# Performance work log

Measured on AMD Instinct MI355X. Metric: run time of the kernel, lower is better.

The kernel has to match this reference:

```python
import jax, jax.numpy as jnp
import numpy as np
from math import comb

N_DERIV = 4          # num_derivatives
ODE_DIM = 512        # ode_dimension
K = ODE_DIM * (N_DERIV + 1)


def _build_system(n, d):
    # system_matrices_1d: A_1d = flip(pascal), Q_1d = flip(hilbert), chol(Q_1d)
    x = np.arange(n + 1)
    B = np.array([[comb(i, j) for j in range(n + 1)] for i in range(n + 1)], dtype=np.float64)
    A1 = B[::-1, ::-1]                                  # flip both axes
    Hil = 1.0 / (x[:, None] + x[None, :] + 1.0)
    Q1 = Hil[::-1, ::-1]
    L1 = np.linalg.cholesky(Q1)
    a = np.kron(np.eye(d), A1)
    q = np.kron(np.eye(d), L1)
    return jnp.asarray(a, jnp.float32), jnp.asarray(q, jnp.float32)


def _qr_r(x):
    # sqrtm_to_cholesky: upper-triangular factor from reduced QR
    return jnp.linalg.qr(x)[1]


def setup_inputs() -> dict:
    key = jax.random.key(0)
    k1, k2, k3, k4, k5 = jax.random.split(key, 5)
    a, q_sqrtm_lower = _build_system(N_DERIV, ODE_DIM)
    m0 = jax.random.normal(k1, (K,), dtype=jnp.float32)
    l0 = jnp.tril(jax.random.normal(k2, (K, K), dtype=jnp.float32) * 0.05)
    H = jax.random.normal(k3, (ODE_DIM, K), dtype=jnp.float32) * 0.1
    bias = jax.random.normal(k4, (ODE_DIM,), dtype=jnp.float32)
    dt = jax.random.uniform(k5, (1,), dtype=jnp.float32, minval=0.05, maxval=0.15)
    return {"m0": m0, "l0": l0, "H": H, "bias": bias, "dt": dt,
            "a": a, "q_sqrtm_lower": q_sqrtm_lower}


def reference(m0, l0, H, bias, dt, a, q_sqrtm_lower):
    d = H.shape[0]
    k = m0.shape[0]
    n1 = k // d                       # num_derivatives + 1
    # --- assemble_preconditioner ---
    powers = jnp.arange(n1 - 1, -1, -1, dtype=m0.dtype)
    scales = jnp.exp(jax.lax.lgamma(powers + 1.0))
    pw = powers + 0.5
    adt = jnp.abs(dt[0])
    p = jnp.tile(adt ** pw / scales, d)          # (k,)
    p_inv = jnp.tile(adt ** (-pw) * scales, d)   # (k,)
    # --- extrapolate_mean ---
    m0_p = p_inv * m0
    m_ext_p = a @ m0_p
    m_ext = p * m_ext_p
    # EK-style linearized observation residual
    m_obs = H @ m_ext - bias                     # (d,)
    # --- estimate_error ---
    l_obs_ns_e = H @ (p_inv[:, None] * q_sqrtm_lower)            # (d,k)
    l_obs_raw = _qr_r(l_obs_ns_e.T).T                            # lower (d,d)
    res_white = jax.scipy.linalg.solve_triangular(l_obs_raw.T, m_obs, lower=False)
    diffusion = jnp.sqrt(jnp.dot(res_white, res_white) / res_white.size)
    error = diffusion * jnp.sqrt(jnp.einsum('nj,nj->n', l_obs_raw, l_obs_raw))
    # --- complete_extrapolation (sum_of_sqrtm_factors) ---
    R1 = (a @ (p_inv[:, None] * l0)).T           # (k,k)
    R2 = (diffusion * q_sqrtm_lower).T           # (k,k)
    l_ext_p = _qr_r(jnp.vstack([R1, R2])).T      # lower (k,k)
    l_ext = p[:, None] * l_ext_p
    # --- final_correction ---
    l_obs_ns = H @ l_ext                         # (d,k)
    l_obs = _qr_r(l_obs_ns.T).T                  # lower (d,d)
    crosscov = l_ext @ l_obs_ns.T                # (k,d)
    gain = jax.scipy.linalg.cho_solve((l_obs, True), crosscov.T).T  # (k,d)
    m_cor = m_ext - gain @ m_obs
    l_cor = l_ext - gain @ l_obs_ns
    u = jnp.reshape(m_cor, (-1, d), order='F')[0]  # derivative-0 block
    return m_cor, l_cor, u, error, diffusion
```

## Files before the change

### kernel.cpp

```cpp
#include <hip/hip_runtime.h>
#include <math.h>

#define KDIM 2560
#define DDIM 512
#define NB 64

#define QM 2560
#define QM2 1024
#define QN 512
#define PW 32
#define UW 3
#define QACT 544

#define OUT_LCOR 2560
#define OUT_U    6556160
#define OUT_ERR  6556672
#define OUT_DIFF 6557184


__global__ void k_setup(const float* dt, double* scal){
  if (threadIdx.x==0 && blockIdx.x==0){
    double adt = fabs((double)dt[0]);
    const double scales[5] = {24.0,6.0,2.0,1.0,1.0};
    for (int i=0;i<5;i++){
      double pw = (double)(4-i)+0.5;
      scal[i]   = pow(adt, pw)/scales[i];
      scal[5+i] = pow(adt,-pw)*scales[i];
    }
  }
}

__global__ __launch_bounds__(256) void k_mext_mobs(const float* a, const float* m0, const float* H,
                                                   const float* bias, const double* scal,
                                                   double* mext, double* mobs){
  __shared__ double me[KDIM];
  __shared__ double red[256];
  double pp[5], pv[5];
  #pragma unroll
  for (int i=0;i<5;i++){ pp[i]=scal[i]; pv[i]=scal[5+i]; }
  int tid=threadIdx.x;
  for (int r=tid; r<KDIM; r+=256){
    int j=r/5, i=r%5;
    const float* arow = a + (size_t)r*KDIM + 5*j;
    const float* m0b  = m0 + 5*j;
    double acc=0;
    #pragma unroll
    for (int l=0;l<5;l++) acc += (double)arow[l]*pv[l]*(double)m0b[l];
    me[r] = pp[i]*acc;
  }
  __syncthreads();
  if (blockIdx.x==0) for (int r=tid;r<KDIM;r+=256) mext[r]=me[r];
  int b = blockIdx.x;
  const float* Hr = H + (size_t)b*KDIM;
  double acc=0;
  for (int c=tid;c<KDIM;c+=256) acc += (double)Hr[c]*me[c];
  red[tid]=acc; __syncthreads();
  for (int s=128;s>0;s>>=1){ if (tid<s) red[tid]+=red[tid+s]; __syncthreads(); }
  if (tid==0) mobs[b] = red[0] - (double)bias[b];
}

__global__ void k_A2(const float* H, const float* q, const double* scal,
                     double* Atop, double* Abot){
  int idx = blockIdx.x*blockDim.x+threadIdx.x;
  if (idx >= QN*QM) return;
  double pv[5];
  #pragma unroll
  for (int t=0;t<5;t++) pv[t]=scal[5+t];
  int j = idx / QM;
  int i = idx % QM;
  int bi = i/5;
  double acc=0;
  #pragma unroll
  for (int t=0;t<5;t++)
    acc += (double)H[(size_t)j*QM + 5*bi+t]*pv[t]*(double)q[(size_t)(5*bi+t)*QM + i];
  if (i < 512) Atop[(size_t)j*QM2 + i] = acc;
  else         Abot[(size_t)j*2048 + (i-512)] = acc;
}

__global__ void k_copyB(const double* Gbot, double* AQ){
  int idx = blockIdx.x*blockDim.x+threadIdx.x;
  if (idx >= 512*512) return;
  int c = idx/512, rr = idx%512;
  AQ[(size_t)c*QM2 + 512 + rr] = (rr<=c) ? Gbot[(size_t)c*512 + rr] : 0.0;
}

__global__ __launch_bounds__(576) void qr_panel(double* A, double* vhead, int col0, double* Tbuf){
  __shared__ double redw[9][PW];
  __shared__ double rednorm[9];
  __shared__ double sh[3];
  __shared__ double wsh[PW];
  __shared__ double alphas[PW], betas[PW];
  __shared__ double VtVs[PW][PW];
  __shared__ double Tsh[PW][PW];
  int tid=threadIdx.x, wid=tid>>6, lane=tid&63;
  int m = QM2 - col0; if (m > QACT) m = QACT;
  bool on = tid < m;
  double x[PW];
  #pragma unroll
  for (int j=0;j<PW;j++)
    x[j] = on ? A[(size_t)(col0+j)*QM2 + col0 + tid] : 0.0;
  for (int j=0;j<PW;j++){
    double v0 = (tid>=j && on)? x[j] : 0.0;
    double ps = v0*v0;
    #pragma unroll
    for (int o=32;o>0;o>>=1) ps += __shfl_down(ps,o);
    if (lane==0) rednorm[wid]=ps;
    if (tid==j) sh[0]=x[j];
    __syncthreads();
    if (tid==0){
      double s0=0;
      for (int t=0;t<9;t++) s0+=rednorm[t];
      double x1=sh[0];
      double nrm=sqrt(s0);
      double alpha=(x1>=0.0)?-nrm:nrm;
      double v1=x1-alpha;
      double vtv=s0-2.0*alpha*x1+alpha*alpha;
      double b=(vtv>0.0)?2.0/vtv:0.0;
      sh[1]=v1; sh[2]=b;
      alphas[j]=alpha; betas[j]=b;
      vhead[col0+j]=v1;
    }
    __syncthreads();
    if (tid==j) x[j]=sh[1];
    double b=sh[2];
    double v=(tid>=j && on)? x[j] : 0.0;
    #pragma unroll
    for (int t=0;t<PW;t++){
      if (t==j) continue;
      double p=v*x[t];
      #pragma unroll
      for (int o=32;o>0;o>>=1) p+=__shfl_down(p,o);
      if (lane==0) redw[wid][t]=p;
    }
    __syncthreads();
    if (tid<PW && tid!=j){
      double tot=0;
      #pragma unroll
      for (int t2=0;t2<9;t2++) tot+=redw[t2][tid];
      if (tid>j) wsh[tid]=b*tot;
      else       VtVs[tid][j]=tot;
    }
    __syncthreads();
    if (v!=0.0){
      for (int t=j+1;t<PW;t++) x[t]-=wsh[t]*v;
    }
  }
  __syncthreads();
  if (tid<PW){
    int i=tid;
    Tsh[i][i]=betas[i];
    for (int j2=i+1;j2<PW;j2++){
      double z=0;
      for (int t=i;t<j2;t++) z+=Tsh[i][t]*VtVs[t][j2];
      Tsh[i][j2]=-betas[j2]*z;
    }
  }
  __syncthreads();
  for (int e=tid;e<PW*PW;e+=576){
    int i=e/PW, j2=e%PW;
    Tbuf[e] = (j2>=i)? Tsh[i][j2] : 0.0;
  }
  if (on){
    #pragma unroll
    for (int j=0;j<PW;j++)
      A[(size_t)(col0+j)*QM2 + col0 + tid] = (tid==j)? alphas[j] : x[j];
  }
}

__global__ __launch_bounds__(256) void qr_update(double* A, const double* vhead,
                                                 const double* Tbuf, int col0){
  __shared__ double redu[4][PW];
  __shared__ double ysh[PW];
  __shared__ double wsh[PW];
  int tid=threadIdx.x, wid=tid>>6, lane=tid&63;
  int cc=col0+PW+blockIdx.x;
  int m=QM2-col0; if (m > QACT) m = QACT;
  double a[UW];
  #pragma unroll
  for (int w=0;w<UW;w++){
    int lr=tid+w*256;
    a[w]=(lr<m)? A[(size_t)cc*QM2+col0+lr] : 0.0;
  }
  double acc[PW];
  #pragma unroll
  for (int j=0;j<PW;j++) acc[j]=0;
  #pragma unroll
  for (int w=0;w<UW;w++){
    int lr=tid+w*256;
    if (lr<m){
      #pragma unroll
      for (int j=0;j<PW;j++){
        double vj;
        if (lr>j)       vj=A[(size_t)(col0+j)*QM2+col0+lr];
        else if (lr==j) vj=vhead[col0+j];
        else            vj=0.0;
        acc[j]+=vj*a[w];
      }
    }
  }
  #pragma unroll
  for (int j=0;j<PW;j++){
    double d=acc[j];
    #pragma unroll
    for (int o=32;o>0;o>>=1) d+=__shfl_down(d,o);
    if (lane==0) redu[wid][j]=d;
  }
  __syncthreads();
  if (tid<PW){
    double y=0;
    #pragma unroll
    for (int t=0;t<4;t++) y+=redu[t][tid];
    ysh[tid]=y;
  }
  __syncthreads();
  if (tid<PW){
    double s=0;
    for (int t=0;t<=tid;t++) s+=Tbuf[t*PW+tid]*ysh[t];
    wsh[tid]=s;
  }
  __syncthreads();
  #pragma unroll
  for (int w=0;w<UW;w++){
    int lr=tid+w*256;
    if (lr<m){
      double s=0;
      #pragma unroll
      for (int j=0;j<PW;j++){
        double vj;
        if (lr>j)       vj=A[(size_t)(col0+j)*QM2+col0+lr];
        else if (lr==j) vj=vhead[col0+j];
        else            vj=0.0;
        s+=vj*wsh[j];
      }
      A[(size_t)cc*QM2+col0+lr]=a[w]-s;
    }
  }
}

__global__ __launch_bounds__(512) void k_rpost(const double* Aq, const double* mobs,
                                               double* scal, float* out){
  __shared__ double b[DDIM];
  __shared__ double xs[DDIM];
  __shared__ double D[NB][NB+1];
  __shared__ double red[DDIM];
  __shared__ double g1sh[DDIM];
  int tid=threadIdx.x;
  {
    double s=0;
    for (int r=0;r<=tid;r++){ double v=Aq[(size_t)tid*QM2 + r]; s+=v*v; }
    g1sh[tid]=s;
  }
  b[tid]=mobs[tid];
  __syncthreads();
  for (int p=7;p>=0;p--){
    int b0=p*NB;
    for (int e=tid;e<NB*NB;e+=512){ int i=e&63, j2=e>>6; D[i][j2]=Aq[(size_t)(b0+j2)*QM2 + b0+i]; }
    __syncthreads();
    if (tid<64){
      double bi=b[b0+tid];
      for (int k=NB-1;k>=0;k--){
        double bk=__shfl(bi,k);
        double xk=bk/D[k][k];
        if (tid<k) bi-=D[tid][k]*xk;
        if (tid==k) bi=xk;
      }
      xs[b0+tid]=bi;
    }
    __syncthreads();
    if (tid<b0){
      double s=0;
      #pragma unroll 8
      for (int j2=0;j2<NB;j2++) s+=Aq[(size_t)(b0+j2)*QM2 + tid]*xs[b0+j2];
      b[tid]-=s;
    }
    __syncthreads();
  }
  red[tid]=xs[tid]*xs[tid]; __syncthreads();
  for (int s=256;s>0;s>>=1){ if (tid<s) red[tid]+=red[tid+s]; __syncthreads(); }
  double diff=sqrt(red[0]/(double)DDIM);
  if (tid==0){ scal[10]=diff; out[OUT_DIFF]=(float)diff; }
  out[OUT_ERR+tid]=(float)(diff*sqrt(fmax(g1sh[tid],0.0)));
}

__global__ void k_X(const float* a, const float* l0, const double* scal, float* X){
  int idx=blockIdx.x*blockDim.x+threadIdx.x;
  if (idx>=KDIM*KDIM) return;
  double pv[5];
  #pragma unroll
  for (int t=0;t<5;t++) pv[t]=scal[5+t];
  int r=idx/KDIM, c=idx%KDIM;
  int j=r/5;
  const float* arow = a + (size_t)r*KDIM + 5*j;
  double acc=0;
  #pragma unroll
  for (int l=0;l<5;l++)
    acc += (double)arow[l]*pv[l]*(double)l0[(size_t)(5*j+l)*KDIM+c];
  X[idx]=(float)acc;
}

template<typename TA,int ATR,typename TB,int BTR,int MODE>
__global__ __launch_bounds__(256) void gemm64(const TA* __restrict__ A,int lda,
                                              const TB* __restrict__ B,int ldb,
                                              void* __restrict__ Cv,int ldc,
                                              int K,int kmode){
  __shared__ double As[16][65];
  __shared__ double Bs[16][65];
  int tid=threadIdx.x, tx=tid&15, ty=tid>>4;
  int n0=blockIdx.x*64, m0=blockIdx.y*64;
  int ks=0, ke=K;
  if (kmode==1) ks=n0;
  else if (kmode==2) ke=min(K,n0+64);
  else if (kmode==3) ke=min(K,m0+64);
  else if (kmode==4) ks=m0;
  double acc[4][4]={};
  for (int k0=ks;k0<ke;k0+=16){
    if (ATR){
      for (int e=tid;e<16*64;e+=256){int k=e>>6,mm=e&63; As[k][mm]=(double)A[(size_t)(k0+k)*lda+m0+mm];}
    } else {
      for (int e=tid;e<64*16;e+=256){int mm=e>>4,k=e&15; As[k][mm]=(double)A[(size_t)(m0+mm)*lda+k0+k];}
    }
    if (BTR){
      for (int e=tid;e<64*16;e+=256){int nn=e>>4,k=e&15; Bs[k][nn]=(double)B[(size_t)(n0+nn)*ldb+k0+k];}
    } else {
      for (int e=tid;e<16*64;e+=256){int k=e>>6,nn=e&63; Bs[k][nn]=(double)B[(size_t)(k0+k)*ldb+n0+nn];}
    }
    __syncthreads();
    #pragma unroll
    for (int t=0;t<16;t++){
      double av[4],bv[4];
      #pragma unroll
      for (int i=0;i<4;i++){av[i]=As[t][ty+16*i];bv[i]=Bs[t][tx+16*i];}
      #pragma unroll
      for (int i=0;i<4;i++)
        #pragma unroll
        for (int j=0;j<4;j++) acc[i][j]+=av[i]*bv[j];
    }
    __syncthreads();
  }
  #pragma unroll
  for (int i=0;i<4;i++){
    #pragma unroll
    for (int j=0;j<4;j++){
      size_t idx=(size_t)(m0+ty+16*i)*ldc+n0+tx+16*j;
      if (MODE==0) ((double*)Cv)[idx]=acc[i][j];
      else if (MODE==1) ((double*)Cv)[idx]-=acc[i][j];
      else ((float*)Cv)[idx]=(float)acc[i][j];
    }
  }
}

__global__ __launch_bounds__(256) void syrk_lower(const float* __restrict__ X, const float* __restrict__ q,
                                                  const double* __restrict__ scal,
                                                  double* __restrict__ G, int n){
  int t = blockIdx.x;
  int u = (int)((sqrtf(8.0f*(float)t+1.0f)+1.0f)*0.5f);
  while ((u*(u-1))/2 > t) u--;
  while ((u*(u+1))/2 <= t) u++;
  int s = (KDIM/64) - u;
  int r = s + (t - (u*(u-1))/2);
  int S0=s*64, R0=r*64;
  __shared__ double As[16][65];
  __shared__ double Bs[16][65];
  int tid=threadIdx.x, tx=tid&15, ty=tid>>4;
  int kend=min(n, S0+80);
  double acc[4][4]={};
  for (int k0=0;k0<kend;k0+=16){
    for (int e=tid;e<64*16;e+=256){int mm=e>>4,k=e&15; As[k][mm]=(double)X[(size_t)(R0+mm)*n+k0+k];}
    for (int e=tid;e<64*16;e+=256){int nn=e>>4,k=e&15; Bs[k][nn]=(double)X[(size_t)(S0+nn)*n+k0+k];}
    __syncthreads();
    #pragma unroll
    for (int t2=0;t2<16;t2++){
      double av[4],bv[4];
      #pragma unroll
      for (int i=0;i<4;i++){av[i]=As[t2][ty+16*i];bv[i]=Bs[t2][tx+16*i];}
      #pragma unroll
      for (int i=0;i<4;i++)
        #pragma unroll
        for (int j=0;j<4;j++) acc[i][j]+=av[i]*bv[j];
    }
    __syncthreads();
  }
  double dd = scal[10]*scal[10];
  #pragma unroll
  for (int i=0;i<4;i++)
    #pragma unroll
    for (int j=0;j<4;j++){
      int rr=R0+ty+16*i, c=S0+tx+16*j;
      double v=acc[i][j];
      if (c<=rr && (rr/5)==(c/5)){
        double qq=0;
        #pragma unroll
        for (int k=0;k<5;k++) qq += (double)q[(size_t)(rr%5)*KDIM+k]*(double)q[(size_t)(c%5)*KDIM+k];
        v += dd*qq;
      }
      G[(size_t)rr*n+c]=v;
    }
}

__global__ __launch_bounds__(256) void chol_diag(double* A, int n, int k0){
  __shared__ double P[NB][NB+1];
  int tid=threadIdx.x;
  for (int e=tid;e<NB*NB;e+=256){int r=e>>6,c=e&63;P[r][c]=A[(size_t)(k0+r)*n+k0+c];}
  int tx=tid&15, ty=tid>>4;
  __syncthreads();
  for (int j=0;j<NB;j++){
    double pj=P[j][j];
    __syncthreads();
    double rpj=1.0/sqrt(fmax(pj,1e-280));
    if (tid>j && tid<NB) P[tid][j]*=rpj;
    if (tid==j) P[j][j]=sqrt(fmax(pj,1e-280));
    __syncthreads();
    #pragma unroll
    for (int a2=0;a2<4;a2++){
      int r=ty+16*a2;
      double lrj=P[r][j];
      #pragma unroll
      for (int b2=0;b2<4;b2++){
        int c=tx+16*b2;
        if (r>j && c>j && c<=r) P[r][c]-=lrj*P[c][j];
      }
    }
    __syncthreads();
  }
  for (int e=tid;e<NB*NB;e+=256){int r=e>>6,c=e&63;A[(size_t)(k0+r)*n+k0+c]=P[r][c];}
}

__global__ __launch_bounds__(256) void chol_trsm(double* A,int n,int k0){
  __shared__ double Ls[NB][NB+1];
  __shared__ double St[NB][NB+1];
  __shared__ double rec[NB];
  int tid=threadIdx.x;
  for (int e=tid;e<NB*NB;e+=256){int r=e>>6,c=e&63;Ls[r][c]=A[(size_t)(k0+r)*n+k0+c];}
  __syncthreads();
  if (tid<NB) rec[tid]=1.0/Ls[tid][tid];
  int base=k0+NB+blockIdx.x*256;
  int myrow=base+tid;
  int mychunk=tid>>6, lrow=tid&63;
  double ar[NB];
  for (int ch=0;ch<4;ch++){
    int r0=base+ch*64;
    for (int e=tid;e<NB*NB;e+=256){
      int r=e>>6,c=e&63;
      if (r0+r<n) St[r][c]=A[(size_t)(r0+r)*n+k0+c];
    }
    __syncthreads();
    if (mychunk==ch && myrow<n){
      #pragma unroll
      for (int c=0;c<NB;c++) ar[c]=St[lrow][c];
    }
    __syncthreads();
  }
  if (myrow<n){
    #pragma unroll
    for (int j=0;j<NB;j++){
      double s=ar[j];
      #pragma unroll
      for (int t=0;t<j;t++) s-=ar[t]*Ls[j][t];
      ar[j]=s*rec[j];
    }
  }
  for (int ch=0;ch<4;ch++){
    int r0=base+ch*64;
    if (mychunk==ch && myrow<n){
      #pragma unroll
      for (int c=0;c<NB;c++) St[lrow][c]=ar[c];
    }
    __syncthreads();
    for (int e=tid;e<NB*NB;e+=256){
      int r=e>>6,c=e&63;
      if (r0+r<n) A[(size_t)(r0+r)*n+k0+c]=St[r][c];
    }
    __syncthreads();
  }
}

__global__ __launch_bounds__(256) void chol_syrk_fd(double* A,int n,int k0){
  int ts0=k0+NB;
  int t=blockIdx.x;
  int r=(int)((sqrtf(8.0f*(float)t+1.0f)-1.0f)*0.5f);
  while ((r*(r+1))/2 > t) r--;
  while (((r+1)*(r+2))/2 <= t) r++;
  int s=t-(r*(r+1))/2;
  int S0=ts0+s*64, R0=ts0+r*64;
  __shared__ double As[16][65];
  __shared__ double Bs[16][65];
  __shared__ double P[NB][NB+1];
  int tid=threadIdx.x, tx=tid&15, ty=tid>>4;
  double acc[4][4]={};
  for (int k0i=0;k0i<NB;k0i+=16){
    for (int e=tid;e<64*16;e+=256){int mm=e>>4,k=e&15; As[k][mm]=A[(size_t)(R0+mm)*n+k0+k0i+k];}
    for (int e=tid;e<64*16;e+=256){int nn=e>>4,k=e&15; Bs[k][nn]=A[(size_t)(S0+nn)*n+k0+k0i+k];}
    __syncthreads();
    #pragma unroll
    for (int tt=0;tt<16;tt++){
      double av[4],bv[4];
      #pragma unroll
      for (int i=0;i<4;i++){av[i]=As[tt][ty+16*i];bv[i]=Bs[tt][tx+16*i];}
      #pragma unroll
      for (int i=0;i<4;i++)
        #pragma unroll
        for (int j=0;j<4;j++) acc[i][j]+=av[i]*bv[j];
    }
    __syncthreads();
  }
  if (t!=0){
    #pragma unroll
    for (int i=0;i<4;i++)
      #pragma unroll
      for (int j=0;j<4;j++)
        A[(size_t)(R0+ty+16*i)*n+S0+tx+16*j]-=acc[i][j];
    return;
  }
  #pragma unroll
  for (int i=0;i<4;i++)
    #pragma unroll
    for (int j=0;j<4;j++)
      P[ty+16*i][tx+16*j] = A[(size_t)(R0+ty+16*i)*n+S0+tx+16*j] - acc[i][j];
  __syncthreads();
  for (int j=0;j<NB;j++){
    double pj=P[j][j];
    __syncthreads();
    double rpj=1.0/sqrt(fmax(pj,1e-280));
    if (tid>j && tid<NB) P[tid][j]*=rpj;
    if (tid==j) P[j][j]=sqrt(fmax(pj,1e-280));
    __syncthreads();
    #pragma unroll
    for (int a2=0;a2<4;a2++){
      int r2=ty+16*a2;
      double lrj=P[r2][j];
      #pragma unroll
      for (int b2=0;b2<4;b2++){
        int c=tx+16*b2;
        if (r2>j && c>j && c<=r2) P[r2][c]-=lrj*P[c][j];
      }
    }
    __syncthreads();
  }
  for (int e=tid;e<NB*NB;e+=256){int r2=e>>6,c=e&63;A[(size_t)(ts0+r2)*n+ts0+c]=P[r2][c];}
}

__global__ void k_extract(const double* G2, const double* scal, float* lext){
  int idx=blockIdx.x*blockDim.x+threadIdx.x;
  if (idx>=KDIM*KDIM) return;
  int r=idx/KDIM, c=idx%KDIM;
  double v = (c<=r)? scal[r%5]*G2[idx] : 0.0;
  lext[idx]=(float)v;
}

__global__ __launch_bounds__(256) void trinv_diag(const double* S, double* Linv){
  __shared__ double Ls[NB][NB+1];
  __shared__ double Ti[NB][NB+1];
  int jb=blockIdx.x, tid=threadIdx.x;
  for (int e=tid; e<DDIM*NB; e+=256){
    int r=e/NB, c=e%NB;
    Linv[(size_t)r*DDIM + jb*NB + c]=0.0;
  }
  for (int e=tid;e<NB*NB;e+=256){int r=e>>6,c=e&63; Ls[r][c]=S[(size_t)(jb*NB+r)*DDIM + jb*NB+c];}
  __syncthreads();
  if (tid<NB){
    int c=tid;
    for (int r=c;r<NB;r++){
      double s=(r==c)?1.0:0.0;
      for (int t=c;t<r;t++) s-=Ls[r][t]*Ti[t][c];
      Ti[r][c]=s/Ls[r][r];
    }
    for (int r=0;r<c;r++) Ti[r][c]=0.0;
  }
  __syncthreads();
  for (int e=tid;e<NB*NB;e+=256){int r=e>>6,c=e&63; Linv[(size_t)(jb*NB+r)*DDIM + jb*NB+c]=Ti[r][c];}
}

__global__ __launch_bounds__(256) void trinv_step(const double* S, double* Linv, int d){
  __shared__ double As[16][65];
  __shared__ double Bs[16][65];
  __shared__ double Ps[NB][NB+1];
  int jb=blockIdx.x, ib=jb+d;
  int tid=threadIdx.x, tx=tid&15, ty=tid>>4;
  double acc[4][4]={};
  int kstart=jb*NB, kend=ib*NB;
  for (int k0=kstart;k0<kend;k0+=16){
    for (int e=tid;e<64*16;e+=256){int mm=e>>4,k=e&15; As[k][mm]=S[(size_t)(ib*NB+mm)*DDIM + k0+k];}
    for (int e=tid;e<16*64;e+=256){int k=e>>6,nn=e&63; Bs[k][nn]=Linv[(size_t)(k0+k)*DDIM + jb*NB+nn];}
    __syncthreads();
    #pragma unroll
    for (int t=0;t<16;t++){
      double av[4],bv[4];
      #pragma unroll
      for (int i=0;i<4;i++){av[i]=As[t][ty+16*i];bv[i]=Bs[t][tx+16*i];}
      #pragma unroll
      for (int i=0;i<4;i++)
        #pragma unroll
        for (int j=0;j<4;j++) acc[i][j]+=av[i]*bv[j];
    }
    __syncthreads();
  }
  #pragma unroll
  for (int i=0;i<4;i++)
    #pragma unroll
    for (int j=0;j<4;j++) Ps[ty+16*i][tx+16*j]=acc[i][j];
  double o[4][4]={};
  __syncthreads();
  for (int k0=0;k0<NB;k0+=16){
    for (int e=tid;e<64*16;e+=256){int mm=e>>4,k=e&15; As[k][mm]=Linv[(size_t)(ib*NB+mm)*DDIM + ib*NB+k0+k];}
    __syncthreads();
    #pragma unroll
    for (int t=0;t<16;t++){
      double av[4],bv[4];
      #pragma unroll
      for (int i=0;i<4;i++){av[i]=As[t][ty+16*i];bv[i]=Ps[k0+t][tx+16*i];}
      #pragma unroll
      for (int i=0;i<4;i++)
        #pragma unroll
        for (int j=0;j<4;j++) o[i][j]+=av[i]*bv[j];
    }
    __syncthreads();
  }
  #pragma unroll
  for (int i=0;i<4;i++)
    #pragma unroll
    for (int j=0;j<4;j++)
      Linv[(size_t)(ib*NB+ty+16*i)*DDIM + jb*NB+tx+16*j] = -o[i][j];
}

__global__ void k_mcor(const double* Z, const double* mobs, const double* mext, float* out){
  __shared__ double mo[DDIM];
  for (int s=threadIdx.x;s<DDIM;s+=256) mo[s]=mobs[s];
  __syncthreads();
  int r=blockIdx.x*256+threadIdx.x;
  if (r>=KDIM) return;
  double acc=0;
  for (int s=0;s<DDIM;s++) acc += Z[(size_t)s*KDIM+r]*mo[s];
  double mc = mext[r]-acc;
  out[r]=(float)mc;
  if (r%5==0) out[OUT_U + r/5]=(float)mc;
}

__global__ __launch_bounds__(256) void k_lcor(const double* __restrict__ Z, const float* __restrict__ lobs,
                                              const float* __restrict__ lext, float* __restrict__ out){
  __shared__ double As[16][65];
  __shared__ double Bs[16][65];
  int tid=threadIdx.x, tx=tid&15, ty=tid>>4;
  int n0=blockIdx.x*64, m0=blockIdx.y*64;
  double acc[4][4]={};
  for (int k0=0;k0<DDIM;k0+=16){
    for (int e=tid;e<16*64;e+=256){int k=e>>6,mm=e&63; As[k][mm]=Z[(size_t)(k0+k)*KDIM+m0+mm];}
    for (int e=tid;e<16*64;e+=256){int k=e>>6,nn=e&63; Bs[k][nn]=(double)lobs[(size_t)(k0+k)*KDIM+n0+nn];}
    __syncthreads();
    #pragma unroll
    for (int t=0;t<16;t++){
      double av[4],bv[4];
      #pragma unroll
      for (int i=0;i<4;i++){av[i]=As[t][ty+16*i];bv[i]=Bs[t][tx+16*i];}
      #pragma unroll
      for (int i=0;i<4;i++)
        #pragma unroll
        for (int j=0;j<4;j++) acc[i][j]+=av[i]*bv[j];
    }
    __syncthreads();
  }
  #pragma unroll
  for (int i=0;i<4;i++)
    #pragma unroll
    for (int j=0;j<4;j++){
      size_t idx=(size_t)(m0+ty+16*i)*KDIM+n0+tx+16*j;
      out[OUT_LCOR+idx]=(float)((double)lext[idx]-acc[i][j]);
    }
}

extern "C" void kernel_launch(void* const* d_in, const int* in_sizes, int n_in,
                              void* d_out, int out_size, void* d_ws, size_t ws_size,
                              hipStream_t stream) {
  const float* m0  = (const float*)d_in[0];
  const float* l0  = (const float*)d_in[1];
  const float* H   = (const float*)d_in[2];
  const float* bias= (const float*)d_in[3];
  const float* dt  = (const float*)d_in[4];
  const float* a   = (const float*)d_in[5];
  const float* q   = (const float*)d_in[6];
  float* out = (float*)d_out;

  char* w=(char*)d_ws;
  auto alloc=[&](size_t bytes)->char*{ char* p=w; w += ((bytes+255)/256)*256; return p; };
  double* scal  =(double*)alloc(16*8);
  double* mext  =(double*)alloc((size_t)KDIM*8);
  double* mobs  =(double*)alloc((size_t)DDIM*8);
  double* vheadA=(double*)alloc((size_t)QN*8);
  double* Tbuf  =(double*)alloc((size_t)PW*PW*8);
  double* AQ    =(double*)alloc((size_t)QM2*QN*8);
  double* S     =(double*)alloc((size_t)DDIM*DDIM*8);
  double* G2    =(double*)alloc((size_t)KDIM*KDIM*8);
  float*  LOBS  =(float*) alloc((size_t)DDIM*KDIM*4);
  float*  X     =(float*) alloc((size_t)KDIM*KDIM*4);
  float*  LEXT  = X;
  double* Abot  = G2;
  double* Gbot  = Abot + (size_t)2048*512;
  double* Linv  = G2;
  double* C2    = Linv + (size_t)DDIM*DDIM;
  double* Y     = C2   + (size_t)DDIM*KDIM;
  double* Z     = Y    + (size_t)DDIM*KDIM;

  auto chol_full=[&](double* M, int n){
    chol_diag<<<1,256,0,stream>>>(M, n, 0);
    for (int k0=0;k0+NB<n;k0+=NB){
      int m = n-k0-NB;
      chol_trsm<<<(m+255)/256,256,0,stream>>>(M,n,k0);
      int T = m/64;
      chol_syrk_fd<<<T*(T+1)/2,256,0,stream>>>(M,n,k0);
    }
  };

  k_setup<<<1,1,0,stream>>>(dt, scal);
  k_mext_mobs<<<DDIM,256,0,stream>>>(a, m0, H, bias, scal, mext, mobs);

  k_A2<<<(QN*QM+255)/256,256,0,stream>>>(H, q, scal, AQ, Abot);
  gemm64<double,0,double,1,0><<<dim3(8,8),256,0,stream>>>(Abot,2048, Abot,2048, Gbot,512, 2048, 0);
  chol_full(Gbot, 512);
  k_copyB<<<(512*512+255)/256,256,0,stream>>>(Gbot, AQ);
  for (int p=0;p<QN/PW;p++){
    int col0=p*PW;
    qr_panel<<<1,576,0,stream>>>(AQ, vheadA, col0, Tbuf);
    int ntr = QN - col0 - PW;
    if (ntr>0) qr_update<<<ntr,256,0,stream>>>(AQ, vheadA, Tbuf, col0);
  }
  k_rpost<<<1,512,0,stream>>>(AQ, mobs, scal, out);

  k_X<<<(KDIM*KDIM+255)/256,256,0,stream>>>(a, l0, scal, X);
  syrk_lower<<<(KDIM/64)*((KDIM/64)+1)/2,256,0,stream>>>(X, q, scal, G2, KDIM);
  chol_full(G2, KDIM);
  k_extract<<<(KDIM*KDIM+255)/256,256,0,stream>>>(G2, scal, LEXT);

  gemm64<float,0,float,0,2><<<dim3(KDIM/64,DDIM/64),256,0,stream>>>(H,KDIM, LEXT,KDIM, LOBS,KDIM, KDIM, 1);
  gemm64<float,0,float,1,0><<<dim3(DDIM/64,DDIM/64),256,0,stream>>>(LOBS,KDIM, LOBS,KDIM, S,DDIM, KDIM, 0);
  chol_full(S, DDIM);
  trinv_diag<<<8,256,0,stream>>>(S, Linv);
  for (int d=1;d<8;d++)
    trinv_step<<<8-d,256,0,stream>>>(S, Linv, d);
  gemm64<float,0,float,1,0><<<dim3(KDIM/64,DDIM/64),256,0,stream>>>(LOBS,KDIM, LEXT,KDIM, C2,KDIM, KDIM, 2);
  gemm64<double,0,double,0,0><<<dim3(KDIM/64,DDIM/64),256,0,stream>>>(Linv,DDIM, C2,KDIM, Y,KDIM, DDIM, 3);
  gemm64<double,1,double,0,0><<<dim3(KDIM/64,DDIM/64),256,0,stream>>>(Linv,DDIM, Y,KDIM, Z,KDIM, DDIM, 4);

  k_mcor<<<(KDIM+255)/256,256,0,stream>>>(Z, mobs, mext, out);
  k_lcor<<<dim3(KDIM/64,KDIM/64),256,0,stream>>>(Z, LOBS, LEXT, out);
}
```

Before: 18.24 ms.

## Fuse blocked QR panel with lookahead trailing update into one launch per step

Replaces the separate qr_panel and qr_update launches with a single qr_step kernel. Block 0 applies the previous panel's reflectors to the next panel and then factors it, while the other blocks update the remaining trailing columns from the previous step, so the panel factorization overlaps with the trailing update. The panel width is halved to 16, which doubles the number of steps but makes each serial panel cheaper. Per-step T factors are kept in a Tbufs array, and the Cholesky syrk kernel gains a fuse flag that is always set to 1, so its behaviour is unchanged.

```diff
diff --git a/kernel.cpp b/kernel.cpp
--- a/kernel.cpp
+++ b/kernel.cpp
@@ -8,9 +8,8 @@
 #define QM 2560
 #define QM2 1024
 #define QN 512
-#define PW 32
-#define UW 3
-#define QACT 544
+#define PW 16
+#define QACT 528
 
 #define OUT_LCOR 2560
 #define OUT_U    6556160
@@ -84,7 +83,60 @@
   AQ[(size_t)c*QM2 + 512 + rr] = (rr<=c) ? Gbot[(size_t)c*512 + rr] : 0.0;
 }
 
-__global__ __launch_bounds__(576) void qr_panel(double* A, double* vhead, int col0, double* Tbuf){
+__global__ __launch_bounds__(576) void qr_step(double* A, double* vhead, double* Tbufs, int p){
+  int col0 = p*PW;
+  int tid=threadIdx.x, wid=tid>>6, lane=tid&63;
+
+  if (blockIdx.x > 0){
+    int pc0 = col0 - PW;
+    const double* T = Tbufs + (size_t)(p-1)*PW*PW;
+    int cc = col0 + PW + ((int)blockIdx.x - 1);
+    int m = QM2 - pc0; if (m>QACT) m=QACT;
+    __shared__ double redu[9][PW];
+    __shared__ double yshu[PW];
+    __shared__ double wshu[PW];
+    int lr = tid;
+    double a = (lr<m)? A[(size_t)cc*QM2 + pc0 + lr] : 0.0;
+    double vv[PW];
+    #pragma unroll
+    for (int j=0;j<PW;j++){
+      double vj=0.0;
+      if (lr<m){
+        if (lr>j)       vj=A[(size_t)(pc0+j)*QM2 + pc0 + lr];
+        else if (lr==j) vj=vhead[pc0+j];
+      }
+      vv[j]=vj;
+    }
+    #pragma unroll
+    for (int j=0;j<PW;j++){
+      double d=vv[j]*a;
+      #pragma unroll
+      for (int o=32;o>0;o>>=1) d+=__shfl_down(d,o);
+      if (lane==0) redu[wid][j]=d;
+    }
+    __syncthreads();
+    if (tid<PW){
+      double y=0;
+      #pragma unroll
+      for (int t=0;t<9;t++) y+=redu[t][tid];
+      yshu[tid]=y;
+    }
+    __syncthreads();
+    if (tid<PW){
+      double s=0;
+      for (int t=0;t<=tid;t++) s+=T[t*PW+tid]*yshu[t];
+      wshu[tid]=s;
+    }
+    __syncthreads();
+    if (lr<m){
+      double s=0;
+      #pragma unroll
+      for (int j=0;j<PW;j++) s+=vv[j]*wshu[j];
+      A[(size_t)cc*QM2 + pc0 + lr]=a-s;
+    }
+    return;
+  }
+
   __shared__ double redw[9][PW];
   __shared__ double rednorm[9];
   __shared__ double sh[3];
@@ -92,13 +144,89 @@
   __shared__ double alphas[PW], betas[PW];
   __shared__ double VtVs[PW][PW];
   __shared__ double Tsh[PW][PW];
-  int tid=threadIdx.x, wid=tid>>6, lane=tid&63;
-  int m = QM2 - col0; if (m > QACT) m = QACT;
+  __shared__ double redP[9][PW*PW];
+  __shared__ double ysh2[PW][PW];
+  __shared__ double wsh2[PW][PW];
+
+  int m = QM2 - col0; if (m>QACT) m=QACT;
   bool on = tid < m;
   double x[PW];
-  #pragma unroll
-  for (int j=0;j<PW;j++)
-    x[j] = on ? A[(size_t)(col0+j)*QM2 + col0 + tid] : 0.0;
+
+  if (p>0){
+    int pc0 = col0 - PW;
+    const double* T = Tbufs + (size_t)(p-1)*PW*PW;
+    int mp = QM2 - pc0; if (mp>QACT) mp=QACT;
+    bool gA = on;
+    bool gB = (tid>=560);
+    int rowA = col0 + tid;
+    int kB   = tid - 560;
+    double vv[PW];
+    #pragma unroll
+    for (int j=0;j<PW;j++){
+      double vj=0.0;
+      if (gA){
+        if (tid + PW < mp) vj = A[(size_t)(pc0+j)*QM2 + rowA];
+      } else if (gB){
+        if (kB>j)       vj=A[(size_t)(pc0+j)*QM2 + pc0 + kB];
+        else if (kB==j) vj=vhead[pc0+j];
+      }
+      vv[j]=vj;
+    }
+    #pragma unroll
+    for (int c=0;c<PW;c++){
+      double a=0.0;
+      if (gA)      a = A[(size_t)(col0+c)*QM2 + rowA];
+      else if (gB) a = A[(size_t)(col0+c)*QM2 + pc0 + kB];
+      x[c]=a;
+    }
+    #pragma unroll
+    for (int c=0;c<PW;c++){
+      #pragma unroll
+      for (int j=0;j<PW;j++){
+        double d=vv[j]*x[c];
+        #pragma unroll
+        for (int o=32;o>0;o>>=1) d+=__shfl_down(d,o);
+        if (lane==0) redP[wid][c*PW+j]=d;
+      }
+    }
+    __syncthreads();
+    if (tid<PW*PW){
+      double y=0;
+      #pragma unroll
+      for (int t=0;t<9;t++) y+=redP[t][tid];
+      ysh2[tid>>4][tid&15]=y;
+    }
+    __syncthreads();
+    if (tid<PW*PW){
+      int c=tid>>4, jj=tid&15;
+      double s=0;
+      for (int t=0;t<=jj;t++) s+=T[t*PW+jj]*ysh2[c][t];
+      wsh2[c][jj]=s;
+    }
+    __syncthreads();
+    #pragma unroll
+    for (int c=0;c<PW;c++){
+      double s=0;
+      #pragma unroll
+      for (int j=0;j<PW;j++) s+=vv[j]*wsh2[c][j];
+      x[c]-=s;
+    }
+    if (gB){
+      #pragma unroll
+      for (int c=0;c<PW;c++) A[(size_t)(col0+c)*QM2 + pc0 + kB] = x[c];
+    }
+    if (!on){
+      #pragma unroll
+      for (int c=0;c<PW;c++) x[c]=0.0;
+    }
+    __syncthreads();
+  } else {
+    #pragma unroll
+    for (int j=0;j<PW;j++)
+      x[j] = on ? A[(size_t)(col0+j)*QM2 + col0 + tid] : 0.0;
+  }
+
+  #pragma unroll
   for (int j=0;j<PW;j++){
     double v0 = (tid>=j && on)? x[j] : 0.0;
     double ps = v0*v0;
@@ -127,10 +255,10 @@
     #pragma unroll
     for (int t=0;t<PW;t++){
       if (t==j) continue;
-      double p=v*x[t];
-      #pragma unroll
-      for (int o=32;o>0;o>>=1) p+=__shfl_down(p,o);
-      if (lane==0) redw[wid][t]=p;
+      double pdot=v*x[t];
+      #pragma unroll
+      for (int o=32;o>0;o>>=1) pdot+=__shfl_down(pdot,o);
+      if (lane==0) redw[wid][t]=pdot;
     }
     __syncthreads();
     if (tid<PW && tid!=j){
@@ -142,6 +270,7 @@
     }
     __syncthreads();
     if (v!=0.0){
+      #pragma unroll
       for (int t=j+1;t<PW;t++) x[t]-=wsh[t]*v;
     }
   }
@@ -158,82 +287,12 @@
   __syncthreads();
   for (int e=tid;e<PW*PW;e+=576){
     int i=e/PW, j2=e%PW;
-    Tbuf[e] = (j2>=i)? Tsh[i][j2] : 0.0;
+    Tbufs[(size_t)p*PW*PW + e] = (j2>=i)? Tsh[i][j2] : 0.0;
   }
   if (on){
     #pragma unroll
     for (int j=0;j<PW;j++)
       A[(size_t)(col0+j)*QM2 + col0 + tid] = (tid==j)? alphas[j] : x[j];
-  }
-}
-
-__global__ __launch_bounds__(256) void qr_update(double* A, const double* vhead,
-                                                 const double* Tbuf, int col0){
-  __shared__ double redu[4][PW];
-  __shared__ double ysh[PW];
-  __shared__ double wsh[PW];
-  int tid=threadIdx.x, wid=tid>>6, lane=tid&63;
-  int cc=col0+PW+blockIdx.x;
-  int m=QM2-col0; if (m > QACT) m = QACT;
-  double a[UW];
-  #pragma unroll
-  for (int w=0;w<UW;w++){
-    int lr=tid+w*256;
-    a[w]=(lr<m)? A[(size_t)cc*QM2+col0+lr] : 0.0;
-  }
-  double acc[PW];
-  #pragma unroll
-  for (int j=0;j<PW;j++) acc[j]=0;
-  #pragma unroll
-  for (int w=0;w<UW;w++){
-    int lr=tid+w*256;
-    if (lr<m){
-      #pragma unroll
-      for (int j=0;j<PW;j++){
-        double vj;
-        if (lr>j)       vj=A[(size_t)(col0+j)*QM2+col0+lr];
-        else if (lr==j) vj=vhead[col0+j];
-        else            vj=0.0;
-        acc[j]+=vj*a[w];
-      }
-    }
-  }
-  #pragma unroll
-  for (int j=0;j<PW;j++){
-    double d=acc[j];
-    #pragma unroll
-    for (int o=32;o>0;o>>=1) d+=__shfl_down(d,o);
-    if (lane==0) redu[wid][j]=d;
-  }
-  __syncthreads();
-  if (tid<PW){
-    double y=0;
-    #pragma unroll
-    for (int t=0;t<4;t++) y+=redu[t][tid];
-    ysh[tid]=y;
-  }
-  __syncthreads();
-  if (tid<PW){
-    double s=0;
-    for (int t=0;t<=tid;t++) s+=Tbuf[t*PW+tid]*ysh[t];
-    wsh[tid]=s;
-  }
-  __syncthreads();
-  #pragma unroll
-  for (int w=0;w<UW;w++){
-    int lr=tid+w*256;
-    if (lr<m){
-      double s=0;
-      #pragma unroll
-      for (int j=0;j<PW;j++){
-        double vj;
-        if (lr>j)       vj=A[(size_t)(col0+j)*QM2+col0+lr];
-        else if (lr==j) vj=vhead[col0+j];
-        else            vj=0.0;
-        s+=vj*wsh[j];
-      }
-      A[(size_t)cc*QM2+col0+lr]=a[w]-s;
-    }
   }
 }
 
@@ -474,7 +533,7 @@
   }
 }
 
-__global__ __launch_bounds__(256) void chol_syrk_fd(double* A,int n,int k0){
+__global__ __launch_bounds__(256) void chol_syrk_fd(double* A,int n,int k0,int fuse){
   int ts0=k0+NB;
   int t=blockIdx.x;
   int r=(int)((sqrtf(8.0f*(float)t+1.0f)-1.0f)*0.5f);
@@ -503,7 +562,7 @@
     }
     __syncthreads();
   }
-  if (t!=0){
+  if (t!=0 || !fuse){
     #pragma unroll
     for (int i=0;i<4;i++)
       #pragma unroll
@@ -685,7 +744,7 @@
   double* mext  =(double*)alloc((size_t)KDIM*8);
   double* mobs  =(double*)alloc((size_t)DDIM*8);
   double* vheadA=(double*)alloc((size_t)QN*8);
-  double* Tbuf  =(double*)alloc((size_t)PW*PW*8);
+  double* Tbufs =(double*)alloc((size_t)(QN/PW)*PW*PW*8);
   double* AQ    =(double*)alloc((size_t)QM2*QN*8);
   double* S     =(double*)alloc((size_t)DDIM*DDIM*8);
   double* G2    =(double*)alloc((size_t)KDIM*KDIM*8);
@@ -705,7 +764,7 @@
       int m = n-k0-NB;
       chol_trsm<<<(m+255)/256,256,0,stream>>>(M,n,k0);
       int T = m/64;
-      chol_syrk_fd<<<T*(T+1)/2,256,0,stream>>>(M,n,k0);
+      chol_syrk_fd<<<T*(T+1)/2,256,0,stream>>>(M,n,k0,1);
     }
   };
 
@@ -717,10 +776,9 @@
   chol_full(Gbot, 512);
   k_copyB<<<(512*512+255)/256,256,0,stream>>>(Gbot, AQ);
   for (int p=0;p<QN/PW;p++){
-    int col0=p*PW;
-    qr_panel<<<1,576,0,stream>>>(AQ, vheadA, col0, Tbuf);
-    int ntr = QN - col0 - PW;
-    if (ntr>0) qr_update<<<ntr,256,0,stream>>>(AQ, vheadA, Tbuf, col0);
+    int nlz = QN - (p+1)*PW;
+    int grid = 1 + ((p>0)? nlz : 0);
+    qr_step<<<grid,576,0,stream>>>(AQ, vheadA, Tbufs, p);
   }
   k_rpost<<<1,512,0,stream>>>(AQ, mobs, scal, out);
 
```

After: 15.73 ms. 13.8% less time.
